# Kernel optimization log

Hardware: AMD Instinct MI355X
Metric: run time of the kernel (lower is better)

## Reference

```python
import jax, jax.numpy as jnp
import numpy as np

VOCAB, DIM, NC, KS, NCLASS = 50000, 300, 256, 3, 3
B, L1, L2 = 128, 512, 32
PAD = (KS - 1) // 2


def setup_inputs() -> dict:
    key = jax.random.key(0)
    ks = jax.random.split(key, 12)
    return {
        "context_ids": jax.random.randint(ks[0], (B, L1), 0, VOCAB),
        "context_masks": jnp.ones((B, L1), jnp.float32),
        "aspect_ids": jax.random.randint(ks[1], (B, L2), 0, VOCAB),
        "aspect_masks": jnp.ones((B, L2), jnp.float32),
        "wordmat": jax.random.normal(ks[2], (VOCAB, DIM), jnp.float32) * 0.1,
        "W": jax.random.normal(ks[3], (DIM, DIM), jnp.float32) * (2.0 / DIM) ** 0.5,
        "ctx_w": jax.random.normal(ks[4], (NC, DIM, KS), jnp.float32) * 0.02,
        "ctx_b": jnp.zeros((NC,), jnp.float32),
        "gate_w": jax.random.normal(ks[5], (NC, 2 * DIM, KS), jnp.float32) * 0.02,
        "gate_b": jnp.zeros((NC,), jnp.float32),
        "lin_w": jax.random.normal(ks[6], (NCLASS, NC), jnp.float32) * 0.05,
        "lin_b": jnp.zeros((NCLASS,), jnp.float32),
    }


def masked_softmax(A, mask):
    # A: (b, l1, l2); mask: (b, l2); normalize over dim=1 (l1), faithful to source
    A_max = jnp.max(A, axis=1, keepdims=True)
    A_exp = jnp.exp(A - A_max) * mask[:, None, :]
    return A_exp / (jnp.sum(A_exp, axis=1, keepdims=True) + 1e-10)


def conv1d(x, w, b):
    # x: (B, C_in, L), w: (C_out, C_in, K) -> (B, C_out, L)
    y = jax.lax.conv_general_dilated(x, w, (1,), [(PAD, PAD)],
                                     dimension_numbers=("NCH", "OIH", "NCH"))
    return y + b[None, :, None]


def reference(context_ids, context_masks, aspect_ids, aspect_masks,
              wordmat, W, ctx_w, ctx_b, gate_w, gate_b, lin_w, lin_b):
    context = wordmat[context_ids]          # (B, L1, D)
    aspect = wordmat[aspect_ids]            # (B, L2, D)
    # FullyAwareAttention
    sx = jax.nn.relu(jnp.einsum("bld,de->ble", context, W))
    sy = jax.nn.relu(jnp.einsum("bld,de->ble", aspect, W))
    s = jnp.einsum("bie,bje->bij", sx, sy)  # (B, L1, L2)
    alpha = masked_softmax(s, aspect_masks)
    att = jnp.einsum("bij,bjd->bid", alpha, aspect)  # (B, L1, D)
    gate_input = jnp.concatenate([context, att], axis=-1)  # (B, L1, 2D)
    sentiment = jnp.tanh(conv1d(context.transpose(0, 2, 1), ctx_w, ctx_b))
    gate = jax.nn.relu(conv1d(gate_input.transpose(0, 2, 1), gate_w, gate_b))
    out = jnp.max(sentiment * gate, axis=2)  # global maxpool over length
    return out @ lin_w.T + lin_b
```

## Files before the change

### kernel.cpp

```cpp
#include <hip/hip_runtime.h>
#include <hip/hip_bf16.h>
#include <math.h>
#include <stdint.h>

#define DIM 300
#define NC 256
#define KS 3
#define NCLASS 3
#define BB 128
#define L1 512
#define L2 32

#define XW 352
#define XROWS 514
#define ROW_B (XW * 2)
#define NKC 11
#define WP2_ELEMS (2 * 4 * 10 * 3 * 4 * 64 * 8)
#define WB_ELEMS (10 * 19 * 64 * 8)
#define WG2_ELEMS (3 * 10 * 16 * 64 * 8)
#define GT_ELEMS (BB * 3 * 32 * 256)
#define GATH_ELEMS (BB * L2 * 320)
#define WAVE_WP_B (10 * 3 * 4 * 1024)

#define ABUF_B 4224
#define EP_LD 516

typedef __attribute__((ext_vector_type(8))) short bf16x8;
typedef __attribute__((ext_vector_type(4))) short bf16x4;
typedef __attribute__((ext_vector_type(4))) float f32x4;

#define GLOBAL_AS __attribute__((address_space(1)))
#define LDS_AS __attribute__((address_space(3)))

__device__ __forceinline__ void gload_lds16(const void* g, void* l) {
    __builtin_amdgcn_global_load_lds((const GLOBAL_AS void*)g, (LDS_AS void*)l, 16, 0, 0);
}

static __device__ __forceinline__ short bfr(float x) {
    __hip_bfloat16 h = __float2bfloat16(x);
    return *(short*)&h;
}

__global__ void prep_all(const float* __restrict__ ctx_w,
                         const float* __restrict__ gate_w,
                         const float* __restrict__ Wm,
                         const int* __restrict__ aids,
                         const float* __restrict__ wordmat,
                         __hip_bfloat16* __restrict__ Wp2,
                         __hip_bfloat16* __restrict__ Wb,
                         __hip_bfloat16* __restrict__ Wg2,
                         __hip_bfloat16* __restrict__ aspb,
                         __hip_bfloat16* __restrict__ syb) {
    int idx = blockIdx.x * 256 + threadIdx.x;
    if (idx < WP2_ELEMS) {
        int jj = idx & 7;
        int lane = (idx >> 3) & 63;
        int n = (idx >> 9) & 3;
        int rest = idx >> 11;
        int tap = rest % 3;
        int r2 = rest / 3;
        int kc = r2 % 10;
        int w = r2 / 10;
        int role = w & 3, cbv = w >> 2;
        int k = kc * 32 + ((lane >> 4) << 3) + jj;
        int nl = role * 64 + n * 16 + (lane & 15);
        float v = 0.f;
        if (nl < 128) {
            int ch = cbv * 128 + nl;
            if (k < 300) v = ctx_w[(ch * DIM + k) * KS + tap];
        } else {
            int ch = cbv * 128 + (nl - 128);
            if (k < 300) v = gate_w[(ch * 2 * DIM + k) * KS + tap];
        }
        Wp2[idx] = __float2bfloat16(v);
        return;
    }
    idx -= WP2_ELEMS;
    if (idx < WB_ELEMS) {
        int j = idx & 7;
        int l = (idx >> 3) & 63;
        int r = idx >> 9;
        int nf = r % 19, kc = r / 19;
        int k = kc * 32 + ((l >> 4) << 3) + j;
        int n = nf * 16 + (l & 15);
        float v = (k < 300 && n < 300) ? Wm[k * DIM + n] : 0.f;
        Wb[idx] = __float2bfloat16(v);
        return;
    }
    idx -= WB_ELEMS;
    if (idx < WG2_ELEMS) {
        int jj = idx & 7;
        int lane = (idx >> 3) & 63;
        int rest = idx >> 9;
        int nf = rest % 16;
        int r2 = rest / 16;
        int kc = r2 % 10, tap = r2 / 10;
        int k = kc * 32 + ((lane >> 4) << 3) + jj;
        int n = nf * 16 + (lane & 15);
        float v = (k < 300) ? gate_w[(n * 2 * DIM + DIM + k) * KS + tap] : 0.f;
        Wg2[idx] = __float2bfloat16(v);
        return;
    }
    idx -= WG2_ELEMS;
    if (idx < GATH_ELEMS) {
        int row = idx / 320, d = idx - row * 320;
        if (d < DIM) {
            aspb[(size_t)row * 320 + d] = __float2bfloat16(wordmat[(size_t)aids[row] * DIM + d]);
        } else {
            aspb[(size_t)row * 320 + d] = __float2bfloat16(0.f);
            if (d >= 304) syb[(size_t)row * 320 + d] = __float2bfloat16(0.f);
        }
    }
}

__global__ __launch_bounds__(256) void xcat_x(const int* __restrict__ cids,
                                              const float* __restrict__ wordmat,
                                              __hip_bfloat16* __restrict__ Xc) {
    int t = threadIdx.x;
    int rloc = t >> 5, lane = t & 31;
    int row = blockIdx.x * 8 + rloc;
    int b = row >> 9, l = row & 511;
    size_t id = (size_t)cids[row];
    const float4* src = (const float4*)(wordmat + id * DIM);
    __hip_bfloat16* dst = Xc + ((size_t)b * XROWS + 1 + l) * XW;
    #pragma unroll
    for (int c = lane; c < 80; c += 32) {
        bf16x4 o;
        if (c < 75) {
            float4 f = src[c];
            o[0] = bfr(f.x); o[1] = bfr(f.y); o[2] = bfr(f.z); o[3] = bfr(f.w);
        } else {
            o = (bf16x4)0;
        }
        ((bf16x4*)dst)[c] = o;
    }
    if (blockIdx.x < 256 && t < 88) {
        int b2 = blockIdx.x >> 1;
        int gr = (blockIdx.x & 1) ? (XROWS - 1) : 0;
        ((bf16x4*)(Xc + ((size_t)b2 * XROWS + gr) * XW))[t] = (bf16x4)0;
    }
}

__global__ __launch_bounds__(256, 2) void asp_mfma(
        const __hip_bfloat16* __restrict__ aspb,
        const __hip_bfloat16* __restrict__ Wb,
        const __hip_bfloat16* __restrict__ Wg2,
        __hip_bfloat16* __restrict__ syb,
        __hip_bfloat16* __restrict__ Gt) {
    const int t = threadIdx.x, wave = t >> 6, l = t & 63;
    const int lane15 = l & 15, lq = l >> 4;
    if (blockIdx.x < 64) {
        const int g = blockIdx.x * 64 + wave * 16 + lane15;
        f32x4 acc[19];
        #pragma unroll
        for (int nf = 0; nf < 19; ++nf) acc[nf] = (f32x4)0.f;
        const bf16x8* Arow = (const bf16x8*)((const char*)aspb + (size_t)g * 640);
        const bf16x8* WbV = (const bf16x8*)Wb;
        for (int kc = 0; kc < 10; ++kc) {
            bf16x8 af = Arow[kc * 4 + lq];
            #pragma unroll
            for (int nf = 0; nf < 19; ++nf)
                acc[nf] = __builtin_amdgcn_mfma_f32_16x16x32_bf16(
                    af, WbV[(kc * 19 + nf) * 64 + l], acc[nf], 0, 0, 0);
        }
        #pragma unroll
        for (int nf = 0; nf < 19; ++nf) {
            int col = nf * 16 + lane15;
            #pragma unroll
            for (int i2 = 0; i2 < 4; ++i2) {
                int row = blockIdx.x * 64 + wave * 16 + lq * 4 + i2;
                syb[(size_t)row * 320 + col] = __float2bfloat16(fmaxf(acc[nf][i2], 0.f));
            }
        }
    } else {
        const int i = blockIdx.x - 64;
        const int b = i / 3, tap = i - b * 3;
        f32x4 acc[2][4];
        #pragma unroll
        for (int m = 0; m < 2; ++m)
            #pragma unroll
            for (int ni = 0; ni < 4; ++ni) acc[m][ni] = (f32x4)0.f;
        const char* Ab = (const char*)aspb + (size_t)b * 32 * 640;
        const bf16x8* WgV = (const bf16x8*)Wg2;
        for (int kc = 0; kc < 10; ++kc) {
            bf16x8 af[2];
            #pragma unroll
            for (int m = 0; m < 2; ++m)
                af[m] = *(const bf16x8*)(Ab + (size_t)(m * 16 + lane15) * 640 + kc * 64 + lq * 16);
            #pragma unroll
            for (int ni = 0; ni < 4; ++ni) {
                bf16x8 bw = WgV[((size_t)(tap * 10 + kc) * 16 + wave * 4 + ni) * 64 + l];
                #pragma unroll
                for (int m = 0; m < 2; ++m)
                    acc[m][ni] = __builtin_amdgcn_mfma_f32_16x16x32_bf16(af[m], bw, acc[m][ni], 0, 0, 0);
            }
        }
        #pragma unroll
        for (int m = 0; m < 2; ++m)
            #pragma unroll
            for (int ni = 0; ni < 4; ++ni) {
                int c = (wave * 4 + ni) * 16 + lane15;
                #pragma unroll
                for (int i2 = 0; i2 < 4; ++i2) {
                    int j = m * 16 + lq * 4 + i2;
                    Gt[((size_t)(b * 3 + tap) * 32 + j) * 256 + c] = __float2bfloat16(acc[m][ni][i2]);
                }
            }
    }
}

__global__ __launch_bounds__(256, 2) void sxs_mfma(
        const __hip_bfloat16* __restrict__ Xc,
        const __hip_bfloat16* __restrict__ Wb,
        const __hip_bfloat16* __restrict__ syb,
        float* __restrict__ s) {
    __shared__ __align__(16) char sxL[4 * 16 * 640];
    const int t = threadIdx.x, wave = t >> 6, l = t & 63;
    const int lane15 = l & 15, lq = l >> 4;
    const int lb = blockIdx.x, b = blockIdx.y;
    const int g = b * XROWS + 1 + lb * 64 + wave * 16 + lane15;

    f32x4 acc[19];
    #pragma unroll
    for (int nf = 0; nf < 19; ++nf) acc[nf] = (f32x4)0.f;

    const bf16x8* Arow = (const bf16x8*)((const char*)Xc + (size_t)g * ROW_B);
    const bf16x8* WbV = (const bf16x8*)Wb;
    for (int kc = 0; kc < 10; ++kc) {
        bf16x8 af = Arow[kc * 4 + lq];
        #pragma unroll
        for (int nf = 0; nf < 19; ++nf)
            acc[nf] = __builtin_amdgcn_mfma_f32_16x16x32_bf16(
                af, WbV[(kc * 19 + nf) * 64 + l], acc[nf], 0, 0, 0);
    }

    char* sxW = sxL + wave * (16 * 640);
    if (l < 32) {
        int row = l >> 1;
        int phys = (2 + (l & 1)) ^ ((row >> 2) & 3);
        *(f32x4*)(sxW + row * 640 + 576 + phys * 16) = (f32x4)0.f;
    }
    #pragma unroll
    for (int nf = 0; nf < 19; ++nf) {
        int col = nf * 16 + lane15;
        #pragma unroll
        for (int i2 = 0; i2 < 4; ++i2) {
            int row = lq * 4 + i2;
            int off = row * 640 + ((col >> 5) << 6) +
                      ((((col >> 3) & 3) ^ ((row >> 2) & 3)) << 4) + ((col & 7) << 1);
            *(__hip_bfloat16*)(sxW + off) = __float2bfloat16(fmaxf(acc[nf][i2], 0.f));
        }
    }
    f32x4 acc2[2];
    acc2[0] = (f32x4)0.f;
    acc2[1] = (f32x4)0.f;
    const bf16x8* syV = (const bf16x8*)syb + (size_t)b * 32 * 40;
    for (int kc = 0; kc < 10; ++kc) {
        bf16x8 af2 = *(const bf16x8*)(sxW + lane15 * 640 + kc * 64 +
                                      ((lq ^ ((lane15 >> 2) & 3)) << 4));
        #pragma unroll
        for (int nj = 0; nj < 2; ++nj) {
            bf16x8 bfj = syV[(nj * 16 + lane15) * 40 + kc * 4 + lq];
            acc2[nj] = __builtin_amdgcn_mfma_f32_16x16x32_bf16(af2, bfj, acc2[nj], 0, 0, 0);
        }
    }
    #pragma unroll
    for (int nj = 0; nj < 2; ++nj)
        #pragma unroll
        for (int i2 = 0; i2 < 4; ++i2) {
            int i = lb * 64 + wave * 16 + lq * 4 + i2;
            s[((size_t)b * L1 + i) * L2 + nj * 16 + lane15] = acc2[nj][i2];
        }
}

__global__ __launch_bounds__(256) void softmax_col(const float* __restrict__ s,
                                                   const float* __restrict__ amask,
                                                   __hip_bfloat16* __restrict__ Xc) {
    __shared__ float red[256];
    __shared__ float cmax[8], cscale[8];
    int b = blockIdx.x, jh = blockIdx.y, t = threadIdx.x;
    int jl = t & 7, j = jh * 8 + jl, ii = t >> 3;
    const float* sb = s + (size_t)b * L1 * L2;
    float v[16];
    float m = -1e30f;
    #pragma unroll
    for (int q = 0; q < 16; ++q) {
        v[q] = sb[(size_t)(ii + q * 32) * L2 + j];
        m = fmaxf(m, v[q]);
    }
    red[t] = m;
    __syncthreads();
    if (t < 8) {
        float mm = red[t];
        for (int p = 1; p < 32; ++p) mm = fmaxf(mm, red[p * 8 + t]);
        cmax[t] = mm;
    }
    __syncthreads();
    float cm = cmax[jl];
    float sum = 0.f;
    #pragma unroll
    for (int q = 0; q < 16; ++q) {
        v[q] = expf(v[q] - cm);
        sum += v[q];
    }
    red[t] = sum;
    __syncthreads();
    if (t < 8) {
        float ss = 0.f;
        for (int p = 0; p < 32; ++p) ss += red[p * 8 + t];
        float mk = amask[b * L2 + jh * 8 + t];
        cscale[t] = mk / (mk * ss + 1e-10f);
    }
    __syncthreads();
    float sc = cscale[jl];
    #pragma unroll
    for (int q = 0; q < 16; ++q) {
        int row = ii + q * 32;
        Xc[((size_t)b * XROWS + 1 + row) * XW + 320 + j] = __float2bfloat16(v[q] * sc);
    }
}

__global__ __launch_bounds__(512, 4) void conv_mfma(
        const __hip_bfloat16* __restrict__ Xc,
        const __hip_bfloat16* __restrict__ Wp2,
        const __hip_bfloat16* __restrict__ Gt,
        const float* __restrict__ ctx_b,
        const float* __restrict__ gate_b,
        float* __restrict__ part) {
    __shared__ __align__(16) char lds[16 * EP_LD * 4];
    const int t = threadIdx.x, wave = t >> 6, lane = t & 63;
    const int lane15 = lane & 15, lq = lane >> 4;
    const int lb = blockIdx.x, b = blockIdx.y, l0 = lb * 64;
    const bool isGate = wave >= 4;
    const int u = isGate ? wave - 4 : wave;
    const int cbv = u >> 1;
    const int role = isGate ? 2 + (u & 1) : (u & 1);

    f32x4 acc[4][4];
    #pragma unroll
    for (int m = 0; m < 4; ++m)
        #pragma unroll
        for (int n = 0; n < 4; ++n) acc[m][n] = (f32x4)0.f;

    const char* XcB = (const char*)Xc + ((size_t)b * XROWS + l0) * ROW_B;
    const char* bbase = (const char*)Wp2 + (size_t)(cbv * 4 + role) * WAVE_WP_B + lane * 16;

    #define STAGE_A(kc_, buf_) do {                                              \
        char* Ab_ = lds + (buf_) * ABUF_B;                                       \
        int chunk = wave * 64 + lane;                                            \
        if (chunk < 264) {                                                       \
            int row_ = chunk >> 2, c_ = chunk & 3;                               \
            int sc_ = (c_ ^ ((row_ >> 1) & 3)) << 4;                             \
            gload_lds16(XcB + (size_t)row_ * ROW_B + (kc_) * 64 + sc_,           \
                        Ab_ + wave * 1024);                                      \
        }                                                                        \
    } while (0)

    STAGE_A(0, 0);
    __syncthreads();

    for (int kc = 0; kc < NKC; ++kc) {
        const int cbuf = kc & 1;
        if (kc < NKC - 1) STAGE_A(kc + 1, cbuf ^ 1);
        const char* Ab = lds + cbuf * ABUF_B;
        if (kc < 10) {
            #pragma unroll
            for (int tap = 0; tap < 3; ++tap) {
                bf16x8 bw[4];
                #pragma unroll
                for (int n = 0; n < 4; ++n)
                    bw[n] = *(const bf16x8*)(bbase + (size_t)((kc * 3 + tap) * 4 + n) * 1024);
                bf16x8 af[4];
                #pragma unroll
                for (int m = 0; m < 4; ++m) {
                    int row = m * 16 + lane15 + tap;
                    af[m] = *(const bf16x8*)(Ab + row * 64 + ((lq ^ ((row >> 1) & 3)) << 4));
                }
                #pragma unroll
                for (int m = 0; m < 4; ++m)
                    #pragma unroll
                    for (int n = 0; n < 4; ++n)
                        acc[m][n] = __builtin_amdgcn_mfma_f32_16x16x32_bf16(
                            af[m], bw[n], acc[m][n], 0, 0, 0);
            }
        } else if (isGate) {
            const char* GtB = (const char*)Gt + (size_t)b * 3 * (32 * 256 * 2);
            #pragma unroll
            for (int tap = 0; tap < 3; ++tap) {
                bf16x8 bw[4];
                #pragma unroll
                for (int n = 0; n < 4; ++n) {
                    #pragma unroll
                    for (int jj = 0; jj < 8; ++jj)
                        ((short*)&bw[n])[jj] = *(const short*)(GtB +
                            (size_t)tap * (32 * 256 * 2) +
                            (size_t)(lq * 8 + jj) * 512 +
                            (size_t)(u * 64 + n * 16 + lane15) * 2);
                }
                bf16x8 af[4];
                #pragma unroll
                for (int m = 0; m < 4; ++m) {
                    int row = m * 16 + lane15 + tap;
                    af[m] = *(const bf16x8*)(Ab + row * 64 + ((lq ^ ((row >> 1) & 3)) << 4));
                }
                #pragma unroll
                for (int m = 0; m < 4; ++m)
                    #pragma unroll
                    for (int n = 0; n < 4; ++n)
                        acc[m][n] = __builtin_amdgcn_mfma_f32_16x16x32_bf16(
                            af[m], bw[n], acc[m][n], 0, 0, 0);
            }
        }
        __syncthreads();
    }
    #undef STAGE_A

    const int cl = t & 255, rh = t >> 8;
    const float bs = ctx_b[cl];
    const float bg = gate_b[cl];
    const int colbase = (isGate ? 256 + u * 64 : u * 64);
    float* ep = (float*)lds;
    float pm = -1e30f;
    for (int ms = 0; ms < 4; ++ms) {
        __syncthreads();
        #pragma unroll
        for (int n = 0; n < 4; ++n) {
            int col = colbase + (n << 4) + lane15;
            #pragma unroll
            for (int i2 = 0; i2 < 4; ++i2)
                ep[(lq * 4 + i2) * EP_LD + col] = acc[ms][n][i2];
        }
        __syncthreads();
        #pragma unroll
        for (int rr = 0; rr < 8; ++rr) {
            int r = rh * 8 + rr;
            float sv = ep[r * EP_LD + cl] + bs;
            float gv = ep[r * EP_LD + 256 + cl] + bg;
            pm = fmaxf(pm, tanhf(sv) * fmaxf(gv, 0.f));
        }
    }
    __syncthreads();
    ep[t] = pm;
    __syncthreads();
    if (t < 256)
        part[((size_t)b * 8 + lb) * 256 + t] = fmaxf(ep[t], ep[t + 256]);
}

__global__ __launch_bounds__(256) void finalize(const float* __restrict__ part,
                                                const float* __restrict__ lin_w,
                                                const float* __restrict__ lin_b,
                                                float* __restrict__ out) {
    __shared__ float pl[256];
    __shared__ float red[256];
    int b = blockIdx.x, t = threadIdx.x;
    float p = part[((size_t)b * 8) * 256 + t];
    for (int lb = 1; lb < 8; ++lb)
        p = fmaxf(p, part[((size_t)b * 8 + lb) * 256 + t]);
    pl[t] = p;
    __syncthreads();
    for (int n = 0; n < NCLASS; ++n) {
        red[t] = pl[t] * lin_w[n * NC + t];
        __syncthreads();
        for (int sft = 128; sft > 0; sft >>= 1) {
            if (t < sft) red[t] += red[t + sft];
            __syncthreads();
        }
        if (t == 0) out[b * NCLASS + n] = red[0] + lin_b[n];
        __syncthreads();
    }
}

extern "C" void kernel_launch(void* const* d_in, const int* in_sizes, int n_in,
                              void* d_out, int out_size, void* d_ws, size_t ws_size,
                              hipStream_t stream) {
    const int* cids = (const int*)d_in[0];
    const int* aids = (const int*)d_in[2];
    const float* amask = (const float*)d_in[3];
    const float* wordmat = (const float*)d_in[4];
    const float* Wm = (const float*)d_in[5];
    const float* ctx_w = (const float*)d_in[6];
    const float* ctx_b = (const float*)d_in[7];
    const float* gate_w = (const float*)d_in[8];
    const float* gate_b = (const float*)d_in[9];
    const float* lin_w = (const float*)d_in[10];
    const float* lin_b = (const float*)d_in[11];
    float* out = (float*)d_out;

    float* sbuf = (float*)d_ws;
    float* part = sbuf + 2097152;
    __hip_bfloat16* aspb = (__hip_bfloat16*)(part + 262144);
    __hip_bfloat16* sybf = aspb + 1310720;
    __hip_bfloat16* Wb   = sybf + 1310720;
    __hip_bfloat16* Wp2  = Wb + WB_ELEMS;
    __hip_bfloat16* Wg2  = Wp2 + WP2_ELEMS;
    __hip_bfloat16* Gt   = Wg2 + WG2_ELEMS;
    __hip_bfloat16* Xc   = Gt + GT_ELEMS;

    const int prepN = WP2_ELEMS + WB_ELEMS + WG2_ELEMS + GATH_ELEMS;
    prep_all<<<(prepN + 255) / 256, 256, 0, stream>>>(ctx_w, gate_w, Wm, aids, wordmat,
                                                      Wp2, Wb, Wg2, aspb, sybf);
    xcat_x<<<BB * L1 / 8, 256, 0, stream>>>(cids, wordmat, Xc);
    asp_mfma<<<64 + BB * 3, 256, 0, stream>>>(aspb, Wb, Wg2, sybf, Gt);
    sxs_mfma<<<dim3(L1 / 64, BB), 256, 0, stream>>>(Xc, Wb, sybf, sbuf);
    softmax_col<<<dim3(BB, 4), 256, 0, stream>>>(sbuf, amask, Xc);
    conv_mfma<<<dim3(8, BB), 512, 0, stream>>>(Xc, Wp2, Gt, ctx_b, gate_b, part);
    finalize<<<BB, 256, 0, stream>>>(part, lin_w, lin_b, out);
}
```

Measured before the change: 171.6 us.

## Merge xcat into prep, split sxs across two kernels, halve conv blocks

```diff
diff --git a/kernel.cpp b/kernel.cpp
--- a/kernel.cpp
+++ b/kernel.cpp
@@ -21,9 +21,11 @@
 #define GT_ELEMS (BB * 3 * 32 * 256)
 #define GATH_ELEMS (BB * L2 * 320)
 #define WAVE_WP_B (10 * 3 * 4 * 1024)
+#define PREP_BLOCKS ((WP2_ELEMS + WB_ELEMS + WG2_ELEMS + GATH_ELEMS) / 256)
+#define XCAT_BLOCKS (BB * L1 / 8)
 
 #define ABUF_B 4224
-#define EP_LD 516
+#define EP_LD1 260
 
 typedef __attribute__((ext_vector_type(8))) short bf16x8;
 typedef __attribute__((ext_vector_type(4))) short bf16x4;
@@ -45,12 +47,41 @@
                          const float* __restrict__ gate_w,
                          const float* __restrict__ Wm,
                          const int* __restrict__ aids,
+                         const int* __restrict__ cids,
                          const float* __restrict__ wordmat,
                          __hip_bfloat16* __restrict__ Wp2,
                          __hip_bfloat16* __restrict__ Wb,
                          __hip_bfloat16* __restrict__ Wg2,
                          __hip_bfloat16* __restrict__ aspb,
-                         __hip_bfloat16* __restrict__ syb) {
+                         __hip_bfloat16* __restrict__ syb,
+                         __hip_bfloat16* __restrict__ Xc) {
+    if (blockIdx.x >= PREP_BLOCKS) {
+        int xb = blockIdx.x - PREP_BLOCKS;
+        int t = threadIdx.x;
+        int rloc = t >> 5, lane = t & 31;
+        int row = xb * 8 + rloc;
+        int b = row >> 9, l = row & 511;
+        size_t id = (size_t)cids[row];
+        const float4* src = (const float4*)(wordmat + id * DIM);
+        __hip_bfloat16* dst = Xc + ((size_t)b * XROWS + 1 + l) * XW;
+        #pragma unroll
+        for (int c = lane; c < 80; c += 32) {
+            bf16x4 o;
+            if (c < 75) {
+                float4 f = src[c];
+                o[0] = bfr(f.x); o[1] = bfr(f.y); o[2] = bfr(f.z); o[3] = bfr(f.w);
+            } else {
+                o = (bf16x4)0;
+            }
+            ((bf16x4*)dst)[c] = o;
+        }
+        if (xb < 256 && t < 88) {
+            int b2 = xb >> 1;
+            int gr = (xb & 1) ? (XROWS - 1) : 0;
+            ((bf16x4*)(Xc + ((size_t)b2 * XROWS + gr) * XW))[t] = (bf16x4)0;
+        }
+        return;
+    }
     int idx = blockIdx.x * 256 + threadIdx.x;
     if (idx < WP2_ELEMS) {
         int jj = idx & 7;
@@ -113,34 +144,6 @@
     }
 }
 
-__global__ __launch_bounds__(256) void xcat_x(const int* __restrict__ cids,
-                                              const float* __restrict__ wordmat,
-                                              __hip_bfloat16* __restrict__ Xc) {
-    int t = threadIdx.x;
-    int rloc = t >> 5, lane = t & 31;
-    int row = blockIdx.x * 8 + rloc;
-    int b = row >> 9, l = row & 511;
-    size_t id = (size_t)cids[row];
-    const float4* src = (const float4*)(wordmat + id * DIM);
-    __hip_bfloat16* dst = Xc + ((size_t)b * XROWS + 1 + l) * XW;
-    #pragma unroll
-    for (int c = lane; c < 80; c += 32) {
-        bf16x4 o;
-        if (c < 75) {
-            float4 f = src[c];
-            o[0] = bfr(f.x); o[1] = bfr(f.y); o[2] = bfr(f.z); o[3] = bfr(f.w);
-        } else {
-            o = (bf16x4)0;
-        }
-        ((bf16x4*)dst)[c] = o;
-    }
-    if (blockIdx.x < 256 && t < 88) {
-        int b2 = blockIdx.x >> 1;
-        int gr = (blockIdx.x & 1) ? (XROWS - 1) : 0;
-        ((bf16x4*)(Xc + ((size_t)b2 * XROWS + gr) * XW))[t] = (bf16x4)0;
-    }
-}
-
 __global__ __launch_bounds__(256, 2) void asp_mfma(
         const __hip_bfloat16* __restrict__ aspb,
         const __hip_bfloat16* __restrict__ Wb,
@@ -273,6 +276,82 @@
         }
 }
 
+__global__ __launch_bounds__(256, 2) void sxs2_mfma(
+        const __hip_bfloat16* __restrict__ Xc,
+        const __hip_bfloat16* __restrict__ Wb,
+        const __hip_bfloat16* __restrict__ syb,
+        float* __restrict__ s) {
+    __shared__ __align__(16) char sxL[4 * 16 * 640];
+    const int t = threadIdx.x, wave = t >> 6, l = t & 63;
+    const int lane15 = l & 15, lq = l >> 4;
+    const int lb = blockIdx.x, b = blockIdx.y + 64;
+    const int r0 = lb * 128 + wave * 16 + lane15;
+
+    f32x4 acc[2][19];
+    #pragma unroll
+    for (int tt = 0; tt < 2; ++tt)
+        #pragma unroll
+        for (int nf = 0; nf < 19; ++nf) acc[tt][nf] = (f32x4)0.f;
+
+    const bf16x8* A0 = (const bf16x8*)((const char*)Xc +
+                       (size_t)(b * XROWS + 1 + r0) * ROW_B);
+    const bf16x8* A1 = (const bf16x8*)((const char*)Xc +
+                       (size_t)(b * XROWS + 1 + r0 + 64) * ROW_B);
+    const bf16x8* WbV = (const bf16x8*)Wb;
+    #pragma unroll 1
+    for (int kc = 0; kc < 10; ++kc) {
+        bf16x8 af0 = A0[kc * 4 + lq];
+        bf16x8 af1 = A1[kc * 4 + lq];
+        #pragma unroll
+        for (int nf = 0; nf < 19; ++nf) {
+            bf16x8 bw = WbV[(kc * 19 + nf) * 64 + l];
+            acc[0][nf] = __builtin_amdgcn_mfma_f32_16x16x32_bf16(af0, bw, acc[0][nf], 0, 0, 0);
+            acc[1][nf] = __builtin_amdgcn_mfma_f32_16x16x32_bf16(af1, bw, acc[1][nf], 0, 0, 0);
+        }
+    }
+
+    char* sxW = sxL + wave * (16 * 640);
+    const bf16x8* syV = (const bf16x8*)syb + (size_t)b * 32 * 40;
+    #pragma unroll
+    for (int tt = 0; tt < 2; ++tt) {
+        if (l < 32) {
+            int row = l >> 1;
+            int phys = (2 + (l & 1)) ^ ((row >> 2) & 3);
+            *(f32x4*)(sxW + row * 640 + 576 + phys * 16) = (f32x4)0.f;
+        }
+        #pragma unroll
+        for (int nf = 0; nf < 19; ++nf) {
+            int col = nf * 16 + lane15;
+            #pragma unroll
+            for (int i2 = 0; i2 < 4; ++i2) {
+                int row = lq * 4 + i2;
+                int off = row * 640 + ((col >> 5) << 6) +
+                          ((((col >> 3) & 3) ^ ((row >> 2) & 3)) << 4) + ((col & 7) << 1);
+                *(__hip_bfloat16*)(sxW + off) = __float2bfloat16(fmaxf(acc[tt][nf][i2], 0.f));
+            }
+        }
+        f32x4 acc2[2];
+        acc2[0] = (f32x4)0.f;
+        acc2[1] = (f32x4)0.f;
+        for (int kc = 0; kc < 10; ++kc) {
+            bf16x8 af2 = *(const bf16x8*)(sxW + lane15 * 640 + kc * 64 +
+                                          ((lq ^ ((lane15 >> 2) & 3)) << 4));
+            #pragma unroll
+            for (int nj = 0; nj < 2; ++nj) {
+                bf16x8 bfj = syV[(nj * 16 + lane15) * 40 + kc * 4 + lq];
+                acc2[nj] = __builtin_amdgcn_mfma_f32_16x16x32_bf16(af2, bfj, acc2[nj], 0, 0, 0);
+            }
+        }
+        #pragma unroll
+        for (int nj = 0; nj < 2; ++nj)
+            #pragma unroll
+            for (int i2 = 0; i2 < 4; ++i2) {
+                int i = lb * 128 + tt * 64 + wave * 16 + lq * 4 + i2;
+                s[((size_t)b * L1 + i) * L2 + nj * 16 + lane15] = acc2[nj][i2];
+            }
+    }
+}
+
 __global__ __launch_bounds__(256) void softmax_col(const float* __restrict__ s,
                                                    const float* __restrict__ amask,
                                                    __hip_bfloat16* __restrict__ Xc) {
@@ -320,21 +399,19 @@
     }
 }
 
-__global__ __launch_bounds__(512, 4) void conv_mfma(
+__global__ __launch_bounds__(256, 4) void conv_v7(
         const __hip_bfloat16* __restrict__ Xc,
         const __hip_bfloat16* __restrict__ Wp2,
         const __hip_bfloat16* __restrict__ Gt,
         const float* __restrict__ ctx_b,
         const float* __restrict__ gate_b,
         float* __restrict__ part) {
-    __shared__ __align__(16) char lds[16 * EP_LD * 4];
+    __shared__ __align__(16) char lds[16 * EP_LD1 * 4];
     const int t = threadIdx.x, wave = t >> 6, lane = t & 63;
     const int lane15 = lane & 15, lq = lane >> 4;
-    const int lb = blockIdx.x, b = blockIdx.y, l0 = lb * 64;
-    const bool isGate = wave >= 4;
-    const int u = isGate ? wave - 4 : wave;
-    const int cbv = u >> 1;
-    const int role = isGate ? 2 + (u & 1) : (u & 1);
+    const int lb = blockIdx.x >> 1, cb = blockIdx.x & 1;
+    const int b = blockIdx.y, l0 = lb * 64;
+    const int role = wave ^ ((blockIdx.x & 1) << 1);
 
     f32x4 acc[4][4];
     #pragma unroll
@@ -343,16 +420,19 @@
         for (int n = 0; n < 4; ++n) acc[m][n] = (f32x4)0.f;
 
     const char* XcB = (const char*)Xc + ((size_t)b * XROWS + l0) * ROW_B;
-    const char* bbase = (const char*)Wp2 + (size_t)(cbv * 4 + role) * WAVE_WP_B + lane * 16;
+    const char* bbase = (const char*)Wp2 + (size_t)(cb * 4 + role) * WAVE_WP_B + lane * 16;
 
     #define STAGE_A(kc_, buf_) do {                                              \
         char* Ab_ = lds + (buf_) * ABUF_B;                                       \
-        int chunk = wave * 64 + lane;                                            \
-        if (chunk < 264) {                                                       \
-            int row_ = chunk >> 2, c_ = chunk & 3;                               \
-            int sc_ = (c_ ^ ((row_ >> 1) & 3)) << 4;                             \
-            gload_lds16(XcB + (size_t)row_ * ROW_B + (kc_) * 64 + sc_,           \
-                        Ab_ + wave * 1024);                                      \
+        _Pragma("unroll")                                                        \
+        for (int i = 0; i < 2; ++i) {                                            \
+            int chunk = (i * 4 + wave) * 64 + lane;                              \
+            if (chunk < 264) {                                                   \
+                int row_ = chunk >> 2, c_ = chunk & 3;                           \
+                int sc_ = (c_ ^ ((row_ >> 1) & 3)) << 4;                         \
+                gload_lds16(XcB + (size_t)row_ * ROW_B + (kc_) * 64 + sc_,       \
+                            Ab_ + (i * 4 + wave) * 1024);                        \
+            }                                                                    \
         }                                                                        \
     } while (0)
 
@@ -383,7 +463,7 @@
                         acc[m][n] = __builtin_amdgcn_mfma_f32_16x16x32_bf16(
                             af[m], bw[n], acc[m][n], 0, 0, 0);
             }
-        } else if (isGate) {
+        } else if (role >= 2) {
             const char* GtB = (const char*)Gt + (size_t)b * 3 * (32 * 256 * 2);
             #pragma unroll
             for (int tap = 0; tap < 3; ++tap) {
@@ -395,7 +475,7 @@
                         ((short*)&bw[n])[jj] = *(const short*)(GtB +
                             (size_t)tap * (32 * 256 * 2) +
                             (size_t)(lq * 8 + jj) * 512 +
-                            (size_t)(u * 64 + n * 16 + lane15) * 2);
+                            (size_t)(cb * 128 + (role & 1) * 64 + n * 16 + lane15) * 2);
                 }
                 bf16x8 af[4];
                 #pragma unroll
@@ -415,35 +495,35 @@
     }
     #undef STAGE_A
 
-    const int cl = t & 255, rh = t >> 8;
-    const float bs = ctx_b[cl];
-    const float bg = gate_b[cl];
-    const int colbase = (isGate ? 256 + u * 64 : u * 64);
+    const int c0 = cb * 128;
+    const int cl = t & 127, rh = t >> 7;
+    const float bs = ctx_b[c0 + cl];
+    const float bg = gate_b[c0 + cl];
     float* ep = (float*)lds;
     float pm = -1e30f;
     for (int ms = 0; ms < 4; ++ms) {
         __syncthreads();
         #pragma unroll
         for (int n = 0; n < 4; ++n) {
-            int col = colbase + (n << 4) + lane15;
+            int col = (role << 6) + (n << 4) + lane15;
             #pragma unroll
             for (int i2 = 0; i2 < 4; ++i2)
-                ep[(lq * 4 + i2) * EP_LD + col] = acc[ms][n][i2];
+                ep[(lq * 4 + i2) * EP_LD1 + col] = acc[ms][n][i2];
         }
         __syncthreads();
         #pragma unroll
         for (int rr = 0; rr < 8; ++rr) {
             int r = rh * 8 + rr;
-            float sv = ep[r * EP_LD + cl] + bs;
-            float gv = ep[r * EP_LD + 256 + cl] + bg;
+            float sv = ep[r * EP_LD1 + cl] + bs;
+            float gv = ep[r * EP_LD1 + 128 + cl] + bg;
             pm = fmaxf(pm, tanhf(sv) * fmaxf(gv, 0.f));
         }
     }
     __syncthreads();
     ep[t] = pm;
     __syncthreads();
-    if (t < 256)
-        part[((size_t)b * 8 + lb) * 256 + t] = fmaxf(ep[t], ep[t + 256]);
+    if (t < 128)
+        part[((size_t)b * 8 + lb) * 256 + c0 + cl] = fmaxf(ep[t], ep[t + 128]);
 }
 
 __global__ __launch_bounds__(256) void finalize(const float* __restrict__ part,
@@ -496,13 +576,12 @@
     __hip_bfloat16* Gt   = Wg2 + WG2_ELEMS;
     __hip_bfloat16* Xc   = Gt + GT_ELEMS;
 
-    const int prepN = WP2_ELEMS + WB_ELEMS + WG2_ELEMS + GATH_ELEMS;
-    prep_all<<<(prepN + 255) / 256, 256, 0, stream>>>(ctx_w, gate_w, Wm, aids, wordmat,
-                                                      Wp2, Wb, Wg2, aspb, sybf);
-    xcat_x<<<BB * L1 / 8, 256, 0, stream>>>(cids, wordmat, Xc);
+    prep_all<<<PREP_BLOCKS + XCAT_BLOCKS, 256, 0, stream>>>(
+        ctx_w, gate_w, Wm, aids, cids, wordmat, Wp2, Wb, Wg2, aspb, sybf, Xc);
     asp_mfma<<<64 + BB * 3, 256, 0, stream>>>(aspb, Wb, Wg2, sybf, Gt);
-    sxs_mfma<<<dim3(L1 / 64, BB), 256, 0, stream>>>(Xc, Wb, sybf, sbuf);
+    sxs_mfma<<<dim3(L1 / 64, 64), 256, 0, stream>>>(Xc, Wb, sybf, sbuf);
+    sxs2_mfma<<<dim3(L1 / 128, 64), 256, 0, stream>>>(Xc, Wb, sybf, sbuf);
     softmax_col<<<dim3(BB, 4), 256, 0, stream>>>(sbuf, amask, Xc);
-    conv_mfma<<<dim3(8, BB), 512, 0, stream>>>(Xc, Wp2, Gt, ctx_b, gate_b, part);
+    conv_v7<<<dim3(16, BB), 256, 0, stream>>>(Xc, Wp2, Gt, ctx_b, gate_b, part);
     finalize<<<BB, 256, 0, stream>>>(part, lin_w, lin_b, out);
 }
```

After: 188.0 us. +9.5%, slower.
